# Kernel tuning notes

Measured on AMD Instinct MI355X. Metric: run time of the kernel, lower is better.

The kernel has to match this reference:

```python
import jax, jax.numpy as jnp
from jax import lax
import numpy as np


def conv4d(x, w, b, pad):
    """4D conv (stride 1) as a sum of 3D convs over the first-spatial-dim kernel taps.
    x: [B, Cin, T, D, H, W]; w: [Cout, Cin, Kt, Kd, Kh, Kw]; same pad on all dims."""
    B, Cin, T, D, H, W = x.shape
    Cout, _, Kt = w.shape[:3]
    xp = jnp.pad(x, ((0, 0), (0, 0), (pad, pad), (0, 0), (0, 0), (0, 0)))
    Tout = T + 2 * pad - Kt + 1
    acc = None
    for k in range(Kt):  # loop over kernel taps (<=3), not data dims
        xs = xp[:, :, k:k + Tout]                      # [B,Cin,Tout,D,H,W]
        xs = xs.transpose(0, 2, 1, 3, 4, 5).reshape(B * Tout, Cin, D, H, W)
        y = lax.conv_general_dilated(
            xs, w[:, :, k], (1, 1, 1), [(pad, pad)] * 3,
            dimension_numbers=('NCDHW', 'OIDHW', 'NCDHW'))
        acc = y if acc is None else acc + y
    Do, Ho, Wo = acc.shape[2:]
    out = acc.reshape(B, Tout, Cout, Do, Ho, Wo).transpose(0, 2, 1, 3, 4, 5)
    return out + b[None, :, None, None, None, None]


def tconv4d_k2s2(x, w, b):
    """4D transposed conv, kernel=2, stride=2, pad=0 (non-overlapping blocks).
    x: [B,Cin,T,D,H,W]; w: [Cin,Cout,2,2,2,2] (PyTorch ConvTranspose layout)."""
    B, Cin, T, D, H, W = x.shape
    Cout = w.shape[1]
    y = jnp.einsum('bcijkl,copqrs->boipjqkrls', x, w)
    y = y.reshape(B, Cout, 2 * T, 2 * D, 2 * H, 2 * W)
    return y + b[None, :, None, None, None, None]


def setup_inputs() -> dict:
    key = jax.random.key(0)
    ks = jax.random.split(key, 10)
    Cin, Cout = 64, 32
    x1 = jax.random.normal(ks[0], (2, Cin, 8, 8, 8, 8), dtype=jnp.float32)
    x2 = jax.random.normal(ks[1], (2, Cin // 2, 16, 16, 16, 16), dtype=jnp.float32)
    def w(k, shape, fan_in):
        return jax.random.normal(k, shape, dtype=jnp.float32) / np.float32(np.sqrt(fan_in))
    up_w = w(ks[2], (Cin, Cin // 2, 2, 2, 2, 2), Cin * 16)
    up_b = w(ks[3], (Cin // 2,), Cin * 16)
    w1 = w(ks[4], (Cout, Cin, 3, 3, 3, 3), Cin * 81)
    b1 = w(ks[5], (Cout,), Cin * 81)
    w2 = w(ks[6], (Cout, Cout, 3, 3, 3, 3), Cout * 81)
    b2 = w(ks[7], (Cout,), Cout * 81)
    w3 = w(ks[8], (Cout, Cin, 1, 1, 1, 1), Cin)
    b3 = w(ks[9], (Cout,), Cin)
    return {'x1': x1, 'x2': x2, 'up_w': up_w, 'up_b': up_b,
            'w1': w1, 'b1': b1, 'w2': w2, 'b2': b2, 'w3': w3, 'b3': b3}


def reference(x1, x2, up_w, up_b, w1, b1, w2, b2, w3, b3):
    x1u = tconv4d_k2s2(x1, up_w, up_b)              # [B, Cin//2, 16,16,16,16]
    xc = jnp.concatenate([x2, x1u], axis=1)          # [B, Cin, 16,16,16,16]
    Y = jax.nn.relu(conv4d(xc, w1, b1, 1))
    Y = conv4d(Y, w2, b2, 1)
    sc = conv4d(xc, w3, b3, 0)                       # 1x1 residual projection
    return jax.nn.relu(Y + sc)
```

## Files before the change

kernel.cpp:

```cpp
#include <hip/hip_runtime.h>

typedef unsigned short u16;
typedef __attribute__((ext_vector_type(8))) short short8;
typedef __attribute__((ext_vector_type(4))) float f32x4;

#define XCB_OFF  0
#define Y1B_OFF  8388608
#define W1P_OFF  12582912
#define W2P_OFF  12748800
#define W3P_OFF  12831744
#define UPWP_OFF 12833792
#define ZPAD_OFF 12866560

__device__ __forceinline__ u16 f2bf(float v) {
    unsigned u = __builtin_bit_cast(unsigned, v);
    u += 0x7FFFu + ((u >> 16) & 1u);
    return (u16)(u >> 16);
}

__device__ __forceinline__ f32x4 MFMA(short8 a, short8 b, f32x4 c) {
    return __builtin_amdgcn_mfma_f32_16x16x32_bf16(a, b, c, 0, 0, 0);
}

typedef const __attribute__((address_space(1))) u16 gas_u16;
typedef __attribute__((address_space(3))) u16 las_u16;
__device__ __forceinline__ void gload16(const u16* g, u16* l) {
    __builtin_amdgcn_global_load_lds((gas_u16*)g, (las_u16*)l, 16, 0, 0);
}

__device__ __forceinline__ void decode_bid(int bid, int& b, int& t, int& d, int& h0) {
    int xcd = bid & 7, loc = bid >> 3;
    int hB = loc & 1;
    d = (loc >> 1) & 15;
    int tsub = (loc >> 5) & 1;
    b = loc >> 6;
    t = xcd * 2 + tsub;
    h0 = hB * 8;
}

__global__ __launch_bounds__(256) void setup(const float* __restrict__ w1,
                                             const float* __restrict__ w2,
                                             const float* __restrict__ w3,
                                             const float* __restrict__ upw,
                                             const float* __restrict__ x2,
                                             u16* __restrict__ ws) {
    __shared__ u16 lds[256 * 40];
    int bid = blockIdx.x;
    int tid = threadIdx.x;
    if (bid == 0 && tid < 64) ws[ZPAD_OFF + tid] = 0;
    if (bid < 512) {
        int b = bid >> 8;
        int pos_base = (bid & 255) * 256;
        u16* xcb = ws + XCB_OFF;
        #pragma unroll
        for (int c = 0; c < 32; ++c) {
            lds[tid * 40 + c] = f2bf(x2[((b * 32 + c) << 16) + pos_base + tid]);
        }
        __syncthreads();
        #pragma unroll
        for (int k = 0; k < 4; ++k) {
            int f = k * 256 + tid;
            int u = f & 3, pos = f >> 2;
            uint4 v = *(const uint4*)(lds + pos * 40 + u * 8);
            *(uint4*)(xcb + (size_t)((b << 16) + pos_base + pos) * 64 + u * 8) = v;
        }
    } else {
        int idx = (bid - 512) * 256 + tid;
        if (idx < 165888) {
            int j = idx & 7, lane = (idx >> 3) & 63, rest = idx >> 9;
            int half = rest & 1, chunk = (rest >> 1) & 1, tap = rest >> 2;
            int co = half * 16 + (lane & 15), ci = chunk * 32 + (lane >> 4) * 8 + j;
            ws[W1P_OFF + idx] = f2bf(w1[(co * 64 + ci) * 81 + tap]);
        } else if (idx < 165888 + 82944) {
            int i2 = idx - 165888;
            int j = i2 & 7, lane = (i2 >> 3) & 63, rest = i2 >> 9;
            int half = rest & 1, tap = rest >> 1;
            int co = half * 16 + (lane & 15), ci = (lane >> 4) * 8 + j;
            ws[W2P_OFF + i2] = f2bf(w2[(co * 32 + ci) * 81 + tap]);
        } else if (idx < 165888 + 82944 + 2048) {
            int i3 = idx - (165888 + 82944);
            int j = i3 & 7, lane = (i3 >> 3) & 63, rest = i3 >> 9;
            int half = rest & 1, chunk = rest >> 1;
            int co = half * 16 + (lane & 15), ci = chunk * 32 + (lane >> 4) * 8 + j;
            ws[W3P_OFF + i3] = f2bf(w3[co * 64 + ci]);
        } else if (idx < 250880 + 32768) {
            int i4 = idx - 250880;
            int j = i4 & 7, lane = (i4 >> 3) & 63, rest = i4 >> 9;
            int half = rest & 1, chunk = (rest >> 1) & 1, tap = rest >> 2;
            int co = half * 16 + (lane & 15), ci = chunk * 32 + (lane >> 4) * 8 + j;
            ws[UPWP_OFF + i4] = f2bf(upw[(ci * 32 + co) * 16 + tap]);
        }
    }
}

__global__ __launch_bounds__(256) void xc_up_mfma(const float* __restrict__ x1,
                                                  const u16* __restrict__ upwp,
                                                  const float* __restrict__ up_b,
                                                  u16* __restrict__ xcb) {
    __shared__ u16 lds[64 * 72];
    int tid = threadIdx.x;
    int wv = tid >> 6, lane = tid & 63;
    int q = lane >> 4, m = lane & 15;
    int bid = blockIdx.x;
    int tp = bid & 1, j = (bid >> 1) & 63, b = bid >> 7;
    int pos_base = j * 64;

    #pragma unroll
    for (int g = 0; g < 16; ++g) {
        int c = g * 4 + wv;
        lds[lane * 72 + c] = f2bf(x1[((b * 64 + c) << 12) + pos_base + lane]);
    }
    __syncthreads();

    const short8* wv8 = (const short8*)upwp;
    float4 bi0 = ((const float4*)up_b)[q];
    float4 bi1 = ((const float4*)up_b)[4 + q];
    int it = j >> 3, id = j & 7;

    for (int tt = 0; tt < 2; ++tt) {
        int tap = tp * 8 + wv * 2 + tt;
        f32x4 acc[4][2];
        #pragma unroll
        for (int g = 0; g < 4; ++g) {
            acc[g][0] = (f32x4){bi0.x, bi0.y, bi0.z, bi0.w};
            acc[g][1] = (f32x4){bi1.x, bi1.y, bi1.z, bi1.w};
        }
        #pragma unroll
        for (int chunk = 0; chunk < 2; ++chunk) {
            short8 a0 = wv8[((tap * 2 + chunk) * 2 + 0) * 64 + lane];
            short8 a1 = wv8[((tap * 2 + chunk) * 2 + 1) * 64 + lane];
            #pragma unroll
            for (int g = 0; g < 4; ++g) {
                short8 bf = *(const short8*)(lds + (g * 16 + m) * 72 + chunk * 32 + q * 8);
                acc[g][0] = MFMA(a0, bf, acc[g][0]);
                acc[g][1] = MFMA(a1, bf, acc[g][1]);
            }
        }
        int pt = tap >> 3, pd = (tap >> 2) & 1, ph = (tap >> 1) & 1, pw = tap & 1;
        int oT = 2 * it + pt, oD = 2 * id + pd, oW = 2 * (m & 7) + pw;
        #pragma unroll
        for (int g = 0; g < 4; ++g) {
            int ih = g * 2 + (m >> 3);
            int opos = oT * 4096 + oD * 256 + (2 * ih + ph) * 16 + oW;
            u16* op = xcb + (size_t)((b << 16) + opos) * 64 + 32 + q * 4;
            #pragma unroll
            for (int half = 0; half < 2; ++half) {
                f32x4 v = acc[g][half];
                uint2 o;
                o.x = (unsigned)f2bf(v.x) | ((unsigned)f2bf(v.y) << 16);
                o.y = (unsigned)f2bf(v.z) | ((unsigned)f2bf(v.w) << 16);
                *(uint2*)(op + half * 16) = o;
            }
        }
    }
}

__global__ __launch_bounds__(256, 3) void conv1_mfma(const u16* __restrict__ xcb,
                                                     const u16* __restrict__ w1p,
                                                     const float* __restrict__ b1,
                                                     const u16* __restrict__ zpad,
                                                     u16* __restrict__ y1b) {
    __shared__ __attribute__((aligned(16))) u16 lds[23040];
    int tid = threadIdx.x;
    int lane = tid & 63, wv = tid >> 6;
    int q = lane >> 4, m = lane & 15;
    int c = wv & 1, rg = wv >> 1;
    int b, t, d, h0;
    decode_bid(blockIdx.x, b, t, d, h0);
    int rot = (blockIdx.x * 5) % 9;

    int gofs[6], lofs[6];
    bool st[6], inr[6];
    #pragma unroll
    for (int k = 0; k < 6; ++k) {
        int ui = tid + k * 256;
        int hh = ui / 144, rem = ui - hh * 144;
        int p = rem >> 3, w = rem & 7;
        int u_src = w ^ (p & 7);
        int gh = h0 - 1 + hh, gw = p - 1;
        st[k] = ui < 1440;
        inr[k] = st[k] && ((unsigned)gh < 16u) && ((unsigned)gw < 16u);
        gofs[k] = (gh * 16 + gw) * 64 + u_src * 8;
        lofs[k] = ui * 8;
    }

    f32x4 acc[4][2];
    if (c == 0) {
        float4 bi0 = ((const float4*)b1)[q];
        float4 bi1 = ((const float4*)b1)[4 + q];
        #pragma unroll
        for (int i = 0; i < 4; ++i) {
            acc[i][0] = (f32x4){bi0.x, bi0.y, bi0.z, bi0.w};
            acc[i][1] = (f32x4){bi1.x, bi1.y, bi1.z, bi1.w};
        }
    } else {
        #pragma unroll
        for (int i = 0; i < 4; ++i) {
            acc[i][0] = (f32x4){0.f, 0.f, 0.f, 0.f};
            acc[i][1] = (f32x4){0.f, 0.f, 0.f, 0.f};
        }
    }
    const short8* w1v = (const short8*)w1p;

    auto issue_plane = [&](int ktd, int bb) {
        int kt = ktd / 3, kd = ktd - kt * 3;
        int tt = t + kt - 1, dd = d + kd - 1;
        bool pv = ((unsigned)tt < 16u) && ((unsigned)dd < 16u);
        const u16* src = xcb + (size_t)(((b * 16 + tt) * 16 + dd)) * 16384;
        #pragma unroll
        for (int k = 0; k < 6; ++k) {
            if (st[k]) {
                const u16* g = (pv && inr[k]) ? (src + gofs[k]) : zpad;
                gload16(g, lds + bb * 11520 + lofs[k]);
            }
        }
    };

    issue_plane(rot, 0);
    for (int s = 0; s < 9; ++s) {
        int ktd = rot + s; if (ktd >= 9) ktd -= 9;
        __syncthreads();
        if (s < 8) {
            int nk = ktd + 1; if (nk >= 9) nk -= 9;
            issue_plane(nk, (s + 1) & 1);
        }
        const u16* L = lds + (s & 1) * 11520;
        __builtin_amdgcn_s_setprio(1);
        #pragma unroll
        for (int kw = 0; kw < 3; ++kw) {
            int p = kw + m, pm = p & 7;
            int bo = p * 64 + ((((c << 2) | q) ^ pm) << 3);
            short8 R[6];
            #pragma unroll
            for (int r = 0; r < 6; ++r)
                R[r] = *(const short8*)(L + (rg * 4 + r) * 1152 + bo);
            #pragma unroll
            for (int kh = 0; kh < 3; ++kh) {
                int tap = (ktd * 3 + kh) * 3 + kw;
                short8 a0 = w1v[((tap * 2 + c) * 2 + 0) * 64 + lane];
                short8 a1 = w1v[((tap * 2 + c) * 2 + 1) * 64 + lane];
                #pragma unroll
                for (int i = 0; i < 4; ++i) {
                    acc[i][0] = MFMA(a0, R[i + kh], acc[i][0]);
                    acc[i][1] = MFMA(a1, R[i + kh], acc[i][1]);
                }
            }
        }
        __builtin_amdgcn_s_setprio(0);
    }

    __syncthreads();
    f32x4* buf = (f32x4*)lds;
    if (c == 1) {
        #pragma unroll
        for (int i = 0; i < 4; ++i)
            #pragma unroll
            for (int half = 0; half < 2; ++half)
                buf[((rg * 4 + i) * 2 + half) * 64 + lane] = acc[i][half];
    }
    __syncthreads();
    if (c == 0) {
        int obase = ((b * 16 + t) * 16 + d) * 256 + (h0 + rg * 4) * 16 + m;
        #pragma unroll
        for (int i = 0; i < 4; ++i) {
            int pos = obase + i * 16;
            #pragma unroll
            for (int half = 0; half < 2; ++half) {
                f32x4 v = acc[i][half];
                f32x4 w = buf[((rg * 4 + i) * 2 + half) * 64 + lane];
                v.x += w.x; v.y += w.y; v.z += w.z; v.w += w.w;
                unsigned r0 = f2bf(fmaxf(v.x, 0.f)), r1 = f2bf(fmaxf(v.y, 0.f));
                unsigned r2 = f2bf(fmaxf(v.z, 0.f)), r3 = f2bf(fmaxf(v.w, 0.f));
                uint2 o;
                o.x = r0 | (r1 << 16);
                o.y = r2 | (r3 << 16);
                *(uint2*)(y1b + (size_t)pos * 32 + half * 16 + q * 4) = o;
            }
        }
    }
}

__global__ __launch_bounds__(256, 3) void conv2_mfma(const u16* __restrict__ y1b,
                                                     const u16* __restrict__ xcb,
                                                     const u16* __restrict__ w2p,
                                                     const u16* __restrict__ w3p,
                                                     const float* __restrict__ b2,
                                                     const float* __restrict__ b3,
                                                     const u16* __restrict__ zpad,
                                                     float* __restrict__ out) {
    __shared__ __attribute__((aligned(16))) u16 lds[20736];
    int tid = threadIdx.x;
    int lane = tid & 63, wv = tid >> 6;
    int q = lane >> 4, m = lane & 15;
    int rg = wv;
    int bid = blockIdx.x;
    int xcd = bid & 7, loc = bid >> 3;
    int d = loc & 15;
    int tsub = (loc >> 4) & 1;
    int b = loc >> 5;
    int t = xcd * 2 + tsub;
    int rot = (bid * 5) % 9;

    int gofs[6], lofs[6];
    bool st[6], inr[6];
    #pragma unroll
    for (int k = 0; k < 6; ++k) {
        int ui = tid + k * 256;
        int hh = ui / 72, rem = ui - hh * 72;
        int p = rem >> 2, w = rem & 3;
        int u_src = w ^ (p & 3);
        int gh = hh - 1, gw = p - 1;
        st[k] = ui < 1296;
        inr[k] = st[k] && ((unsigned)gh < 16u) && ((unsigned)gw < 16u);
        gofs[k] = (gh * 16 + gw) * 32 + u_src * 8;
        lofs[k] = ui * 8;
    }

    f32x4 acc[4][2];
    #pragma unroll
    for (int hf = 0; hf < 2; ++hf) {
        float4 p0 = ((const float4*)b2)[hf * 4 + q];
        float4 s0 = ((const float4*)b3)[hf * 4 + q];
        #pragma unroll
        for (int i = 0; i < 4; ++i)
            acc[i][hf] = (f32x4){p0.x + s0.x, p0.y + s0.y, p0.z + s0.z, p0.w + s0.w};
    }
    const short8* w2v = (const short8*)w2p;

    auto issue_plane = [&](int ktd, int bb) {
        int kt = ktd / 3, kd = ktd - kt * 3;
        int tt = t + kt - 1, dd = d + kd - 1;
        bool pv = ((unsigned)tt < 16u) && ((unsigned)dd < 16u);
        const u16* src = y1b + (size_t)(((b * 16 + tt) * 16 + dd)) * 8192;
        #pragma unroll
        for (int k = 0; k < 6; ++k) {
            if (st[k]) {
                const u16* g = (pv && inr[k]) ? (src + gofs[k]) : zpad;
                gload16(g, lds + bb * 10368 + lofs[k]);
            }
        }
    };

    issue_plane(rot, 0);
    for (int s = 0; s < 9; ++s) {
        int ktd = rot + s; if (ktd >= 9) ktd -= 9;
        __syncthreads();
        if (s < 8) {
            int nk = ktd + 1; if (nk >= 9) nk -= 9;
            issue_plane(nk, (s + 1) & 1);
        }
        const u16* L = lds + (s & 1) * 10368;
        __builtin_amdgcn_s_setprio(1);
        #pragma unroll
        for (int kw = 0; kw < 3; ++kw) {
            int p = kw + m, pm = p & 3;
            int bo = p * 32 + ((q ^ pm) << 3);
            short8 R[6];
            #pragma unroll
            for (int r = 0; r < 6; ++r)
                R[r] = *(const short8*)(L + (rg * 4 + r) * 576 + bo);
            #pragma unroll
            for (int kh = 0; kh < 3; ++kh) {
                int tap = (ktd * 3 + kh) * 3 + kw;
                short8 a0 = w2v[(tap * 2 + 0) * 64 + lane];
                short8 a1 = w2v[(tap * 2 + 1) * 64 + lane];
                #pragma unroll
                for (int i = 0; i < 4; ++i) {
                    acc[i][0] = MFMA(a0, R[i + kh], acc[i][0]);
                    acc[i][1] = MFMA(a1, R[i + kh], acc[i][1]);
                }
            }
        }
        __builtin_amdgcn_s_setprio(0);
    }

    const short8* w3v = (const short8*)w3p;
    int lpos0 = (t * 16 + d) * 256 + (rg * 4) * 16 + m;
    int gpos0 = (b << 16) + lpos0;
    #pragma unroll
    for (int chunk = 0; chunk < 2; ++chunk) {
        short8 a0 = w3v[(chunk * 2 + 0) * 64 + lane];
        short8 a1 = w3v[(chunk * 2 + 1) * 64 + lane];
        #pragma unroll
        for (int i = 0; i < 4; ++i) {
            short8 bf = *(const short8*)(xcb + (size_t)(gpos0 + i * 16) * 64 + ((chunk << 2) | q) * 8);
            acc[i][0] = MFMA(a0, bf, acc[i][0]);
            acc[i][1] = MFMA(a1, bf, acc[i][1]);
        }
    }

    #pragma unroll
    for (int i = 0; i < 4; ++i) {
        int lpos = lpos0 + i * 16;
        #pragma unroll
        for (int hf = 0; hf < 2; ++hf) {
            f32x4 v = acc[i][hf];
            int co = hf * 16 + q * 4;
            float* op = out + (((size_t)(b * 32 + co)) << 16) + lpos;
            op[0ull << 16] = fmaxf(v.x, 0.f);
            op[1ull << 16] = fmaxf(v.y, 0.f);
            op[2ull << 16] = fmaxf(v.z, 0.f);
            op[3ull << 16] = fmaxf(v.w, 0.f);
        }
    }
}

extern "C" void kernel_launch(void* const* d_in, const int* in_sizes, int n_in,
                              void* d_out, int out_size, void* d_ws, size_t ws_size,
                              hipStream_t stream) {
    const float* x1   = (const float*)d_in[0];
    const float* x2   = (const float*)d_in[1];
    const float* up_w = (const float*)d_in[2];
    const float* up_b = (const float*)d_in[3];
    const float* w1   = (const float*)d_in[4];
    const float* b1   = (const float*)d_in[5];
    const float* w2   = (const float*)d_in[6];
    const float* b2   = (const float*)d_in[7];
    const float* w3   = (const float*)d_in[8];
    const float* b3   = (const float*)d_in[9];
    u16* ws  = (u16*)d_ws;
    float* out = (float*)d_out;

    setup<<<1620, 256, 0, stream>>>(w1, w2, w3, up_w, x2, ws);
    xc_up_mfma<<<256, 256, 0, stream>>>(x1, ws + UPWP_OFF, up_b, ws + XCB_OFF);
    conv1_mfma<<<1024, 256, 0, stream>>>(ws + XCB_OFF, ws + W1P_OFF, b1,
                                         ws + ZPAD_OFF, ws + Y1B_OFF);
    conv2_mfma<<<512, 256, 0, stream>>>(ws + Y1B_OFF, ws + XCB_OFF, ws + W2P_OFF,
                                        ws + W3P_OFF, b2, b3, ws + ZPAD_OFF, out);
}
```

Before: 162.9 us.

## Compute two output T slices per conv1 block to reuse loaded input planes

Each conv1 block now produces two adjacent T output slices, streaming 12 input planes and applying the matching kernel T-tap to each output's accumulator set. This cuts redundant global-to-LDS plane loads from 18 to 12 per output pair and halves the grid. In exchange it doubles accumulator registers, lowers the occupancy hint to 2 blocks per CU, and launches fewer blocks, which may reduce latency hiding.

```diff
diff --git a/kernel.cpp b/kernel.cpp
--- a/kernel.cpp
+++ b/kernel.cpp
@@ -26,16 +26,6 @@
 typedef __attribute__((address_space(3))) u16 las_u16;
 __device__ __forceinline__ void gload16(const u16* g, u16* l) {
     __builtin_amdgcn_global_load_lds((gas_u16*)g, (las_u16*)l, 16, 0, 0);
-}
-
-__device__ __forceinline__ void decode_bid(int bid, int& b, int& t, int& d, int& h0) {
-    int xcd = bid & 7, loc = bid >> 3;
-    int hB = loc & 1;
-    d = (loc >> 1) & 15;
-    int tsub = (loc >> 5) & 1;
-    b = loc >> 6;
-    t = xcd * 2 + tsub;
-    h0 = hB * 8;
 }
 
 __global__ __launch_bounds__(256) void setup(const float* __restrict__ w1,
@@ -155,7 +145,7 @@
     }
 }
 
-__global__ __launch_bounds__(256, 3) void conv1_mfma(const u16* __restrict__ xcb,
+__global__ __launch_bounds__(256, 2) void conv1_mfma(const u16* __restrict__ xcb,
                                                      const u16* __restrict__ w1p,
                                                      const float* __restrict__ b1,
                                                      const u16* __restrict__ zpad,
@@ -165,9 +155,13 @@
     int lane = tid & 63, wv = tid >> 6;
     int q = lane >> 4, m = lane & 15;
     int c = wv & 1, rg = wv >> 1;
-    int b, t, d, h0;
-    decode_bid(blockIdx.x, b, t, d, h0);
-    int rot = (blockIdx.x * 5) % 9;
+    int bid = blockIdx.x;
+    int tp = bid & 7, loc = bid >> 3;
+    int hB = loc & 1;
+    int d = (loc >> 1) & 15;
+    int b = (loc >> 5) & 1;
+    int t0 = tp * 2, h0 = hB * 8;
+    int rot = (bid * 5) % 12;
 
     int gofs[6], lofs[6];
     bool st[6], inr[6];
@@ -184,27 +178,31 @@
         lofs[k] = ui * 8;
     }
 
-    f32x4 acc[4][2];
+    f32x4 acc[2][4][2];
     if (c == 0) {
         float4 bi0 = ((const float4*)b1)[q];
         float4 bi1 = ((const float4*)b1)[4 + q];
         #pragma unroll
-        for (int i = 0; i < 4; ++i) {
-            acc[i][0] = (f32x4){bi0.x, bi0.y, bi0.z, bi0.w};
-            acc[i][1] = (f32x4){bi1.x, bi1.y, bi1.z, bi1.w};
-        }
+        for (int jt = 0; jt < 2; ++jt)
+            #pragma unroll
+            for (int i = 0; i < 4; ++i) {
+                acc[jt][i][0] = (f32x4){bi0.x, bi0.y, bi0.z, bi0.w};
+                acc[jt][i][1] = (f32x4){bi1.x, bi1.y, bi1.z, bi1.w};
+            }
     } else {
         #pragma unroll
-        for (int i = 0; i < 4; ++i) {
-            acc[i][0] = (f32x4){0.f, 0.f, 0.f, 0.f};
-            acc[i][1] = (f32x4){0.f, 0.f, 0.f, 0.f};
-        }
+        for (int jt = 0; jt < 2; ++jt)
+            #pragma unroll
+            for (int i = 0; i < 4; ++i) {
+                acc[jt][i][0] = (f32x4){0.f, 0.f, 0.f, 0.f};
+                acc[jt][i][1] = (f32x4){0.f, 0.f, 0.f, 0.f};
+            }
     }
     const short8* w1v = (const short8*)w1p;
 
-    auto issue_plane = [&](int ktd, int bb) {
-        int kt = ktd / 3, kd = ktd - kt * 3;
-        int tt = t + kt - 1, dd = d + kd - 1;
+    auto issue_plane = [&](int pl, int bb) {
+        int kt4 = pl / 3, kd = pl - kt4 * 3;
+        int tt = t0 - 1 + kt4, dd = d - 1 + kd;
         bool pv = ((unsigned)tt < 16u) && ((unsigned)dd < 16u);
         const u16* src = xcb + (size_t)(((b * 16 + tt) * 16 + dd)) * 16384;
         #pragma unroll
@@ -217,14 +215,15 @@
     };
 
     issue_plane(rot, 0);
-    for (int s = 0; s < 9; ++s) {
-        int ktd = rot + s; if (ktd >= 9) ktd -= 9;
+    for (int s = 0; s < 12; ++s) {
+        int pl = rot + s; if (pl >= 12) pl -= 12;
         __syncthreads();
-        if (s < 8) {
-            int nk = ktd + 1; if (nk >= 9) nk -= 9;
-            issue_plane(nk, (s + 1) & 1);
+        if (s < 11) {
+            int np = pl + 1; if (np >= 12) np -= 12;
+            issue_plane(np, (s + 1) & 1);
         }
         const u16* L = lds + (s & 1) * 11520;
+        int kt4 = pl / 3, kd = pl - kt4 * 3;
         __builtin_amdgcn_s_setprio(1);
         #pragma unroll
         for (int kw = 0; kw < 3; ++kw) {
@@ -234,15 +233,30 @@
             #pragma unroll
             for (int r = 0; r < 6; ++r)
                 R[r] = *(const short8*)(L + (rg * 4 + r) * 1152 + bo);
-            #pragma unroll
-            for (int kh = 0; kh < 3; ++kh) {
-                int tap = (ktd * 3 + kh) * 3 + kw;
-                short8 a0 = w1v[((tap * 2 + c) * 2 + 0) * 64 + lane];
-                short8 a1 = w1v[((tap * 2 + c) * 2 + 1) * 64 + lane];
+            if (kt4 <= 2) {
                 #pragma unroll
-                for (int i = 0; i < 4; ++i) {
-                    acc[i][0] = MFMA(a0, R[i + kh], acc[i][0]);
-                    acc[i][1] = MFMA(a1, R[i + kh], acc[i][1]);
+                for (int kh = 0; kh < 3; ++kh) {
+                    int tap = ((kt4 * 3 + kd) * 3 + kh) * 3 + kw;
+                    short8 a0 = w1v[((tap * 2 + c) * 2 + 0) * 64 + lane];
+                    short8 a1 = w1v[((tap * 2 + c) * 2 + 1) * 64 + lane];
+                    #pragma unroll
+                    for (int i = 0; i < 4; ++i) {
+                        acc[0][i][0] = MFMA(a0, R[i + kh], acc[0][i][0]);
+                        acc[0][i][1] = MFMA(a1, R[i + kh], acc[0][i][1]);
+                    }
+                }
+            }
+            if (kt4 >= 1) {
+                #pragma unroll
+                for (int kh = 0; kh < 3; ++kh) {
+                    int tap = (((kt4 - 1) * 3 + kd) * 3 + kh) * 3 + kw;
+                    short8 a0 = w1v[((tap * 2 + c) * 2 + 0) * 64 + lane];
+                    short8 a1 = w1v[((tap * 2 + c) * 2 + 1) * 64 + lane];
+                    #pragma unroll
+                    for (int i = 0; i < 4; ++i) {
+                        acc[1][i][0] = MFMA(a0, R[i + kh], acc[1][i][0]);
+                        acc[1][i][1] = MFMA(a1, R[i + kh], acc[1][i][1]);
+                    }
                 }
             }
         }
@@ -253,28 +267,33 @@
     f32x4* buf = (f32x4*)lds;
     if (c == 1) {
         #pragma unroll
-        for (int i = 0; i < 4; ++i)
-            #pragma unroll
-            for (int half = 0; half < 2; ++half)
-                buf[((rg * 4 + i) * 2 + half) * 64 + lane] = acc[i][half];
+        for (int jt = 0; jt < 2; ++jt)
+            #pragma unroll
+            for (int i = 0; i < 4; ++i)
+                #pragma unroll
+                for (int half = 0; half < 2; ++half)
+                    buf[((jt * 8 + rg * 4 + i) * 2 + half) * 64 + lane] = acc[jt][i][half];
     }
     __syncthreads();
     if (c == 0) {
-        int obase = ((b * 16 + t) * 16 + d) * 256 + (h0 + rg * 4) * 16 + m;
-        #pragma unroll
-        for (int i = 0; i < 4; ++i) {
-            int pos = obase + i * 16;
-            #pragma unroll
-            for (int half = 0; half < 2; ++half) {
-                f32x4 v = acc[i][half];
-                f32x4 w = buf[((rg * 4 + i) * 2 + half) * 64 + lane];
-                v.x += w.x; v.y += w.y; v.z += w.z; v.w += w.w;
-                unsigned r0 = f2bf(fmaxf(v.x, 0.f)), r1 = f2bf(fmaxf(v.y, 0.f));
-                unsigned r2 = f2bf(fmaxf(v.z, 0.f)), r3 = f2bf(fmaxf(v.w, 0.f));
-                uint2 o;
-                o.x = r0 | (r1 << 16);
-                o.y = r2 | (r3 << 16);
-                *(uint2*)(y1b + (size_t)pos * 32 + half * 16 + q * 4) = o;
+        #pragma unroll
+        for (int jt = 0; jt < 2; ++jt) {
+            int obase = ((b * 16 + t0 + jt) * 16 + d) * 256 + (h0 + rg * 4) * 16 + m;
+            #pragma unroll
+            for (int i = 0; i < 4; ++i) {
+                int pos = obase + i * 16;
+                #pragma unroll
+                for (int half = 0; half < 2; ++half) {
+                    f32x4 v = acc[jt][i][half];
+                    f32x4 w = buf[((jt * 8 + rg * 4 + i) * 2 + half) * 64 + lane];
+                    v.x += w.x; v.y += w.y; v.z += w.z; v.w += w.w;
+                    unsigned r0 = f2bf(fmaxf(v.x, 0.f)), r1 = f2bf(fmaxf(v.y, 0.f));
+                    unsigned r2 = f2bf(fmaxf(v.z, 0.f)), r3 = f2bf(fmaxf(v.w, 0.f));
+                    uint2 o;
+                    o.x = r0 | (r1 << 16);
+                    o.y = r2 | (r3 << 16);
+                    *(uint2*)(y1b + (size_t)pos * 32 + half * 16 + q * 4) = o;
+                }
             }
         }
     }
@@ -423,8 +442,8 @@
 
     setup<<<1620, 256, 0, stream>>>(w1, w2, w3, up_w, x2, ws);
     xc_up_mfma<<<256, 256, 0, stream>>>(x1, ws + UPWP_OFF, up_b, ws + XCB_OFF);
-    conv1_mfma<<<1024, 256, 0, stream>>>(ws + XCB_OFF, ws + W1P_OFF, b1,
-                                         ws + ZPAD_OFF, ws + Y1B_OFF);
+    conv1_mfma<<<512, 256, 0, stream>>>(ws + XCB_OFF, ws + W1P_OFF, b1,
+                                        ws + ZPAD_OFF, ws + Y1B_OFF);
     conv2_mfma<<<512, 256, 0, stream>>>(ws + Y1B_OFF, ws + XCB_OFF, ws + W2P_OFF,
                                         ws + W3P_OFF, b2, b3, ws + ZPAD_OFF, out);
 }
```

Result: no change. 162.8 us (-0.0%).

## Enlarge conv1 block tile to two d-slices by full H, drop split-K reduction

Applied to the files above, without the earlier changes.

conv1 now assigns each block a full 16x16 HW plane for two adjacent d outputs. It streams 12 input planes (3 t by 4 d) through double-buffered LDS, and each wave handles one d-slice and 8 H rows across all 64 input channels. This replaces the previous split of the channel reduction across waves and the LDS reduction epilogue. Neighbouring d outputs reuse the same loaded planes, which cuts redundant global loads. The trade-off is a 4x smaller grid (256 blocks), twice the LDS, and more accumulator registers, which lowers occupancy. Each wave also sits idle on a quarter of the planes, and conv2's block-to-XCD mapping is rearranged to match.

```diff
diff --git a/kernel.cpp b/kernel.cpp
--- a/kernel.cpp
+++ b/kernel.cpp
@@ -26,16 +26,6 @@
 typedef __attribute__((address_space(3))) u16 las_u16;
 __device__ __forceinline__ void gload16(const u16* g, u16* l) {
     __builtin_amdgcn_global_load_lds((gas_u16*)g, (las_u16*)l, 16, 0, 0);
-}
-
-__device__ __forceinline__ void decode_bid(int bid, int& b, int& t, int& d, int& h0) {
-    int xcd = bid & 7, loc = bid >> 3;
-    int hB = loc & 1;
-    d = (loc >> 1) & 15;
-    int tsub = (loc >> 5) & 1;
-    b = loc >> 6;
-    t = xcd * 2 + tsub;
-    h0 = hB * 8;
 }
 
 __global__ __launch_bounds__(256) void setup(const float* __restrict__ w1,
@@ -155,127 +145,119 @@
     }
 }
 
-__global__ __launch_bounds__(256, 3) void conv1_mfma(const u16* __restrict__ xcb,
-                                                     const u16* __restrict__ w1p,
-                                                     const float* __restrict__ b1,
-                                                     const u16* __restrict__ zpad,
-                                                     u16* __restrict__ y1b) {
-    __shared__ __attribute__((aligned(16))) u16 lds[23040];
+__global__ __launch_bounds__(256) void conv1_mfma(const u16* __restrict__ xcb,
+                                                  const u16* __restrict__ w1p,
+                                                  const float* __restrict__ b1,
+                                                  const u16* __restrict__ zpad,
+                                                  u16* __restrict__ y1b) {
+    __shared__ __attribute__((aligned(16))) u16 lds[41472];
     int tid = threadIdx.x;
     int lane = tid & 63, wv = tid >> 6;
     int q = lane >> 4, m = lane & 15;
-    int c = wv & 1, rg = wv >> 1;
-    int b, t, d, h0;
-    decode_bid(blockIdx.x, b, t, d, h0);
-    int rot = (blockIdx.x * 5) % 9;
-
-    int gofs[6], lofs[6];
-    bool st[6], inr[6];
-    #pragma unroll
-    for (int k = 0; k < 6; ++k) {
+    int dlt = wv & 1, rh = wv >> 1;
+    int bid = blockIdx.x;
+    int xcd = bid & 7;
+    int b = xcd >> 2, tq = xcd & 3;
+    int loc = bid >> 3;
+    int dp = loc & 7;
+    int tl = (loc >> 3) & 3;
+    int t = tq * 4 + tl;
+    int d0 = dp * 2;
+    int rot = (bid * 5) % 12;
+
+    int gofs[11], lofs[11];
+    bool st[11], inr[11];
+    #pragma unroll
+    for (int k = 0; k < 11; ++k) {
         int ui = tid + k * 256;
-        int hh = ui / 144, rem = ui - hh * 144;
-        int p = rem >> 3, w = rem & 7;
-        int u_src = w ^ (p & 7);
-        int gh = h0 - 1 + hh, gw = p - 1;
-        st[k] = ui < 1440;
+        int u = ui & 7, col = (ui >> 3) % 18, row = ui / 144;
+        int u_src = u ^ (col & 7);
+        int gh = row - 1, gw = col - 1;
+        st[k] = ui < 2592;
         inr[k] = st[k] && ((unsigned)gh < 16u) && ((unsigned)gw < 16u);
         gofs[k] = (gh * 16 + gw) * 64 + u_src * 8;
         lofs[k] = ui * 8;
     }
 
-    f32x4 acc[4][2];
-    if (c == 0) {
+    f32x4 acc[8][2];
+    {
         float4 bi0 = ((const float4*)b1)[q];
         float4 bi1 = ((const float4*)b1)[4 + q];
         #pragma unroll
-        for (int i = 0; i < 4; ++i) {
+        for (int i = 0; i < 8; ++i) {
             acc[i][0] = (f32x4){bi0.x, bi0.y, bi0.z, bi0.w};
             acc[i][1] = (f32x4){bi1.x, bi1.y, bi1.z, bi1.w};
         }
-    } else {
-        #pragma unroll
-        for (int i = 0; i < 4; ++i) {
-            acc[i][0] = (f32x4){0.f, 0.f, 0.f, 0.f};
-            acc[i][1] = (f32x4){0.f, 0.f, 0.f, 0.f};
-        }
     }
     const short8* w1v = (const short8*)w1p;
 
-    auto issue_plane = [&](int ktd, int bb) {
-        int kt = ktd / 3, kd = ktd - kt * 3;
-        int tt = t + kt - 1, dd = d + kd - 1;
+    auto issue_plane = [&](int pl, int bb) {
+        int kt = pl >> 2, dd4 = pl & 3;
+        int tt = t - 1 + kt, dd = d0 - 1 + dd4;
         bool pv = ((unsigned)tt < 16u) && ((unsigned)dd < 16u);
         const u16* src = xcb + (size_t)(((b * 16 + tt) * 16 + dd)) * 16384;
         #pragma unroll
-        for (int k = 0; k < 6; ++k) {
+        for (int k = 0; k < 11; ++k) {
             if (st[k]) {
                 const u16* g = (pv && inr[k]) ? (src + gofs[k]) : zpad;
-                gload16(g, lds + bb * 11520 + lofs[k]);
+                gload16(g, lds + bb * 20736 + lofs[k]);
             }
         }
     };
 
     issue_plane(rot, 0);
-    for (int s = 0; s < 9; ++s) {
-        int ktd = rot + s; if (ktd >= 9) ktd -= 9;
+    for (int s = 0; s < 12; ++s) {
+        int pl = rot + s; if (pl >= 12) pl -= 12;
         __syncthreads();
-        if (s < 8) {
-            int nk = ktd + 1; if (nk >= 9) nk -= 9;
-            issue_plane(nk, (s + 1) & 1);
-        }
-        const u16* L = lds + (s & 1) * 11520;
-        __builtin_amdgcn_s_setprio(1);
-        #pragma unroll
-        for (int kw = 0; kw < 3; ++kw) {
-            int p = kw + m, pm = p & 7;
-            int bo = p * 64 + ((((c << 2) | q) ^ pm) << 3);
-            short8 R[6];
+        if (s < 11) {
+            int np = pl + 1; if (np >= 12) np -= 12;
+            issue_plane(np, (s + 1) & 1);
+        }
+        const u16* L = lds + (s & 1) * 20736;
+        int kt = pl >> 2, dd4 = pl & 3;
+        int kd = dd4 - dlt;
+        if ((unsigned)kd <= 2u) {
+            __builtin_amdgcn_s_setprio(1);
             #pragma unroll
-            for (int r = 0; r < 6; ++r)
-                R[r] = *(const short8*)(L + (rg * 4 + r) * 1152 + bo);
-            #pragma unroll
-            for (int kh = 0; kh < 3; ++kh) {
-                int tap = (ktd * 3 + kh) * 3 + kw;
-                short8 a0 = w1v[((tap * 2 + c) * 2 + 0) * 64 + lane];
-                short8 a1 = w1v[((tap * 2 + c) * 2 + 1) * 64 + lane];
+            for (int kw = 0; kw < 3; ++kw) {
+                int p = kw + m, pm = p & 7;
                 #pragma unroll
-                for (int i = 0; i < 4; ++i) {
-                    acc[i][0] = MFMA(a0, R[i + kh], acc[i][0]);
-                    acc[i][1] = MFMA(a1, R[i + kh], acc[i][1]);
+                for (int chunk = 0; chunk < 2; ++chunk) {
+                    int bo = p * 64 + ((((chunk << 2) | q) ^ pm) << 3);
+                    short8 R[10];
+                    #pragma unroll
+                    for (int r = 0; r < 10; ++r)
+                        R[r] = *(const short8*)(L + (rh * 8 + r) * 1152 + bo);
+                    #pragma unroll
+                    for (int kh = 0; kh < 3; ++kh) {
+                        int tap = ((kt * 3 + kd) * 3 + kh) * 3 + kw;
+                        short8 a0 = w1v[((tap * 2 + chunk) * 2 + 0) * 64 + lane];
+                        short8 a1 = w1v[((tap * 2 + chunk) * 2 + 1) * 64 + lane];
+                        #pragma unroll
+                        for (int i = 0; i < 8; ++i) {
+                            acc[i][0] = MFMA(a0, R[i + kh], acc[i][0]);
+                            acc[i][1] = MFMA(a1, R[i + kh], acc[i][1]);
+                        }
+                    }
                 }
             }
-        }
-        __builtin_amdgcn_s_setprio(0);
-    }
-
-    __syncthreads();
-    f32x4* buf = (f32x4*)lds;
-    if (c == 1) {
-        #pragma unroll
-        for (int i = 0; i < 4; ++i)
-            #pragma unroll
-            for (int half = 0; half < 2; ++half)
-                buf[((rg * 4 + i) * 2 + half) * 64 + lane] = acc[i][half];
-    }
-    __syncthreads();
-    if (c == 0) {
-        int obase = ((b * 16 + t) * 16 + d) * 256 + (h0 + rg * 4) * 16 + m;
-        #pragma unroll
-        for (int i = 0; i < 4; ++i) {
-            int pos = obase + i * 16;
-            #pragma unroll
-            for (int half = 0; half < 2; ++half) {
-                f32x4 v = acc[i][half];
-                f32x4 w = buf[((rg * 4 + i) * 2 + half) * 64 + lane];
-                v.x += w.x; v.y += w.y; v.z += w.z; v.w += w.w;
-                unsigned r0 = f2bf(fmaxf(v.x, 0.f)), r1 = f2bf(fmaxf(v.y, 0.f));
-                unsigned r2 = f2bf(fmaxf(v.z, 0.f)), r3 = f2bf(fmaxf(v.w, 0.f));
-                uint2 o;
-                o.x = r0 | (r1 << 16);
-                o.y = r2 | (r3 << 16);
-                *(uint2*)(y1b + (size_t)pos * 32 + half * 16 + q * 4) = o;
-            }
+            __builtin_amdgcn_s_setprio(0);
+        }
+    }
+
+    int obase = ((b * 16 + t) * 16 + d0 + dlt) * 256 + (rh * 8) * 16 + m;
+    #pragma unroll
+    for (int i = 0; i < 8; ++i) {
+        int pos = obase + i * 16;
+        #pragma unroll
+        for (int half = 0; half < 2; ++half) {
+            f32x4 v = acc[i][half];
+            unsigned r0 = f2bf(fmaxf(v.x, 0.f)), r1 = f2bf(fmaxf(v.y, 0.f));
+            unsigned r2 = f2bf(fmaxf(v.z, 0.f)), r3 = f2bf(fmaxf(v.w, 0.f));
+            uint2 o;
+            o.x = r0 | (r1 << 16);
+            o.y = r2 | (r3 << 16);
+            *(uint2*)(y1b + (size_t)pos * 32 + half * 16 + q * 4) = o;
         }
     }
 }
@@ -294,11 +276,12 @@
     int q = lane >> 4, m = lane & 15;
     int rg = wv;
     int bid = blockIdx.x;
-    int xcd = bid & 7, loc = bid >> 3;
+    int xcd = bid & 7;
+    int b = xcd >> 2, tq = xcd & 3;
+    int loc = bid >> 3;
     int d = loc & 15;
-    int tsub = (loc >> 4) & 1;
-    int b = loc >> 5;
-    int t = xcd * 2 + tsub;
+    int tl = (loc >> 4) & 3;
+    int t = tq * 4 + tl;
     int rot = (bid * 5) % 9;
 
     int gofs[6], lofs[6];
@@ -423,8 +406,8 @@
 
     setup<<<1620, 256, 0, stream>>>(w1, w2, w3, up_w, x2, ws);
     xc_up_mfma<<<256, 256, 0, stream>>>(x1, ws + UPWP_OFF, up_b, ws + XCB_OFF);
-    conv1_mfma<<<1024, 256, 0, stream>>>(ws + XCB_OFF, ws + W1P_OFF, b1,
-                                         ws + ZPAD_OFF, ws + Y1B_OFF);
+    conv1_mfma<<<256, 256, 0, stream>>>(ws + XCB_OFF, ws + W1P_OFF, b1,
+                                        ws + ZPAD_OFF, ws + Y1B_OFF);
     conv2_mfma<<<512, 256, 0, stream>>>(ws + Y1B_OFF, ws + XCB_OFF, ws + W2P_OFF,
                                         ws + W3P_OFF, b2, b3, ws + ZPAD_OFF, out);
 }
```

After: 176.4 us. +8.3%, slower.

## Prefetch per-plane weights into registers, remap blocks to XCDs by batch/time-quarter

Applied to the files above, without the earlier changes.

Both conv kernels now load all 18 weight fragments for the current kernel plane into registers at the top of each stage, before issuing the next plane's async LDS loads. Scheduling barriers keep those weight loads from being interleaved with the MFMA loop. Block-to-XCD mapping changes so each XCD owns one batch and a quarter of T, which is meant to improve L2 reuse of neighbouring planes. The extra register pressure lowers the launch-bounds occupancy hint from 3 to 2, and conv1's LDS array grows with a larger stride between its two buffers.

```diff
diff --git a/kernel.cpp b/kernel.cpp
--- a/kernel.cpp
+++ b/kernel.cpp
@@ -26,16 +26,6 @@
 typedef __attribute__((address_space(3))) u16 las_u16;
 __device__ __forceinline__ void gload16(const u16* g, u16* l) {
     __builtin_amdgcn_global_load_lds((gas_u16*)g, (las_u16*)l, 16, 0, 0);
-}
-
-__device__ __forceinline__ void decode_bid(int bid, int& b, int& t, int& d, int& h0) {
-    int xcd = bid & 7, loc = bid >> 3;
-    int hB = loc & 1;
-    d = (loc >> 1) & 15;
-    int tsub = (loc >> 5) & 1;
-    b = loc >> 6;
-    t = xcd * 2 + tsub;
-    h0 = hB * 8;
 }
 
 __global__ __launch_bounds__(256) void setup(const float* __restrict__ w1,
@@ -155,19 +145,26 @@
     }
 }
 
-__global__ __launch_bounds__(256, 3) void conv1_mfma(const u16* __restrict__ xcb,
+__global__ __launch_bounds__(256, 2) void conv1_mfma(const u16* __restrict__ xcb,
                                                      const u16* __restrict__ w1p,
                                                      const float* __restrict__ b1,
                                                      const u16* __restrict__ zpad,
                                                      u16* __restrict__ y1b) {
-    __shared__ __attribute__((aligned(16))) u16 lds[23040];
+    __shared__ __attribute__((aligned(16))) u16 lds[27648];
     int tid = threadIdx.x;
     int lane = tid & 63, wv = tid >> 6;
     int q = lane >> 4, m = lane & 15;
     int c = wv & 1, rg = wv >> 1;
-    int b, t, d, h0;
-    decode_bid(blockIdx.x, b, t, d, h0);
-    int rot = (blockIdx.x * 5) % 9;
+    int bid = blockIdx.x;
+    int xcd = bid & 7;
+    int b = xcd >> 2, tq = xcd & 3;
+    int loc = bid >> 3;
+    int hB = loc & 1;
+    int d = (loc >> 1) & 15;
+    int tl = (loc >> 5) & 3;
+    int t = tq * 4 + tl;
+    int h0 = hB * 8;
+    int rot = (bid * 5) % 9;
 
     int gofs[6], lofs[6];
     bool st[6], inr[6];
@@ -211,7 +208,7 @@
         for (int k = 0; k < 6; ++k) {
             if (st[k]) {
                 const u16* g = (pv && inr[k]) ? (src + gofs[k]) : zpad;
-                gload16(g, lds + bb * 11520 + lofs[k]);
+                gload16(g, lds + bb * 13824 + lofs[k]);
             }
         }
     };
@@ -219,12 +216,24 @@
     issue_plane(rot, 0);
     for (int s = 0; s < 9; ++s) {
         int ktd = rot + s; if (ktd >= 9) ktd -= 9;
+        int kt = ktd / 3, kd = ktd - kt * 3;
         __syncthreads();
+        short8 W[3][3][2];
+        #pragma unroll
+        for (int kw = 0; kw < 3; ++kw)
+            #pragma unroll
+            for (int kh = 0; kh < 3; ++kh) {
+                int tap = ((kt * 3 + kd) * 3 + kh) * 3 + kw;
+                W[kw][kh][0] = w1v[((tap * 2 + c) * 2 + 0) * 64 + lane];
+                W[kw][kh][1] = w1v[((tap * 2 + c) * 2 + 1) * 64 + lane];
+            }
+        __builtin_amdgcn_sched_barrier(0);
         if (s < 8) {
             int nk = ktd + 1; if (nk >= 9) nk -= 9;
             issue_plane(nk, (s + 1) & 1);
         }
-        const u16* L = lds + (s & 1) * 11520;
+        __builtin_amdgcn_sched_barrier(0);
+        const u16* L = lds + (s & 1) * 13824;
         __builtin_amdgcn_s_setprio(1);
         #pragma unroll
         for (int kw = 0; kw < 3; ++kw) {
@@ -236,13 +245,10 @@
                 R[r] = *(const short8*)(L + (rg * 4 + r) * 1152 + bo);
             #pragma unroll
             for (int kh = 0; kh < 3; ++kh) {
-                int tap = (ktd * 3 + kh) * 3 + kw;
-                short8 a0 = w1v[((tap * 2 + c) * 2 + 0) * 64 + lane];
-                short8 a1 = w1v[((tap * 2 + c) * 2 + 1) * 64 + lane];
                 #pragma unroll
                 for (int i = 0; i < 4; ++i) {
-                    acc[i][0] = MFMA(a0, R[i + kh], acc[i][0]);
-                    acc[i][1] = MFMA(a1, R[i + kh], acc[i][1]);
+                    acc[i][0] = MFMA(W[kw][kh][0], R[i + kh], acc[i][0]);
+                    acc[i][1] = MFMA(W[kw][kh][1], R[i + kh], acc[i][1]);
                 }
             }
         }
@@ -280,7 +286,7 @@
     }
 }
 
-__global__ __launch_bounds__(256, 3) void conv2_mfma(const u16* __restrict__ y1b,
+__global__ __launch_bounds__(256, 2) void conv2_mfma(const u16* __restrict__ y1b,
                                                      const u16* __restrict__ xcb,
                                                      const u16* __restrict__ w2p,
                                                      const u16* __restrict__ w3p,
@@ -294,11 +300,12 @@
     int q = lane >> 4, m = lane & 15;
     int rg = wv;
     int bid = blockIdx.x;
-    int xcd = bid & 7, loc = bid >> 3;
+    int xcd = bid & 7;
+    int b = xcd >> 2, tq = xcd & 3;
+    int loc = bid >> 3;
     int d = loc & 15;
-    int tsub = (loc >> 4) & 1;
-    int b = loc >> 5;
-    int t = xcd * 2 + tsub;
+    int tl = (loc >> 4) & 3;
+    int t = tq * 4 + tl;
     int rot = (bid * 5) % 9;
 
     int gofs[6], lofs[6];
@@ -345,10 +352,21 @@
     for (int s = 0; s < 9; ++s) {
         int ktd = rot + s; if (ktd >= 9) ktd -= 9;
         __syncthreads();
+        short8 W[3][3][2];
+        #pragma unroll
+        for (int kw = 0; kw < 3; ++kw)
+            #pragma unroll
+            for (int kh = 0; kh < 3; ++kh) {
+                int tap = (ktd * 3 + kh) * 3 + kw;
+                W[kw][kh][0] = w2v[(tap * 2 + 0) * 64 + lane];
+                W[kw][kh][1] = w2v[(tap * 2 + 1) * 64 + lane];
+            }
+        __builtin_amdgcn_sched_barrier(0);
         if (s < 8) {
             int nk = ktd + 1; if (nk >= 9) nk -= 9;
             issue_plane(nk, (s + 1) & 1);
         }
+        __builtin_amdgcn_sched_barrier(0);
         const u16* L = lds + (s & 1) * 10368;
         __builtin_amdgcn_s_setprio(1);
         #pragma unroll
@@ -361,13 +379,10 @@
                 R[r] = *(const short8*)(L + (rg * 4 + r) * 576 + bo);
             #pragma unroll
             for (int kh = 0; kh < 3; ++kh) {
-                int tap = (ktd * 3 + kh) * 3 + kw;
-                short8 a0 = w2v[(tap * 2 + 0) * 64 + lane];
-                short8 a1 = w2v[(tap * 2 + 1) * 64 + lane];
                 #pragma unroll
                 for (int i = 0; i < 4; ++i) {
-                    acc[i][0] = MFMA(a0, R[i + kh], acc[i][0]);
-                    acc[i][1] = MFMA(a1, R[i + kh], acc[i][1]);
+                    acc[i][0] = MFMA(W[kw][kh][0], R[i + kh], acc[i][0]);
+                    acc[i][1] = MFMA(W[kw][kh][1], R[i + kh], acc[i][1]);
                 }
             }
         }
```

New measurement: 155.9 us. -4.3%, faster.
